# Optimization experiments

Hardware: AMD Instinct MI355X
Metric: run time of the kernel (lower is better)

Reference implementation:

```python
import jax, jax.numpy as jnp
import numpy as np

B, S, D, H = 4, 2048, 1024, 16
HD = D // H  # head dim = 64


def setup_inputs() -> dict:
    key = jax.random.key(0)
    ks = jax.random.split(key, 6)
    hidden_states = jax.random.normal(ks[0], (B, S, D), dtype=jnp.float32)
    attention_mask = jnp.zeros((B, S), dtype=bool)  # ignored by the module (set to None in forward)
    # RoPE cache: standard rotary angles per position
    inv_freq = 1.0 / (10000.0 ** (jnp.arange(0, HD, 2, dtype=jnp.float32) / HD))  # [HD/2]
    ang = jnp.arange(S, dtype=jnp.float32)[:, None] * inv_freq[None, :]  # [S, HD/2]
    ang = jnp.concatenate([ang, ang], axis=-1)  # [S, HD]
    rope_cos = jnp.cos(ang)
    rope_sin = jnp.sin(ang)
    scale = 1.0 / np.sqrt(D)
    Wq = jax.random.normal(ks[1], (D, D), dtype=jnp.float32) * scale
    Wk = jax.random.normal(ks[2], (D, D), dtype=jnp.float32) * scale
    Wv = jax.random.normal(ks[3], (D, D), dtype=jnp.float32) * scale
    return {"hidden_states": hidden_states, "attention_mask": attention_mask,
            "rope_cos": rope_cos, "rope_sin": rope_sin, "Wq": Wq, "Wk": Wk, "Wv": Wv}


def _rotate_half(x):
    x1, x2 = jnp.split(x, 2, axis=-1)
    return jnp.concatenate([-x2, x1], axis=-1)


def _apply_rope(x, cos, sin):
    # x: [B, H, S, HD]; cos/sin: [S, HD]
    return x * cos[None, None, :, :] + _rotate_half(x) * sin[None, None, :, :]


def reference(hidden_states, attention_mask, rope_cos, rope_sin, Wq, Wk, Wv):
    del attention_mask  # forward() sets attention_mask = None
    b, s, d = hidden_states.shape
    # QKV projections (nn.Linear: y = x @ W.T), split into heads -> [B, H, S, HD]
    def proj(W):
        y = jnp.einsum('bsd,ed->bse', hidden_states, W)
        return y.reshape(b, s, H, HD).transpose(0, 2, 1, 3)
    q = _apply_rope(proj(Wq), rope_cos, rope_sin)
    k = _apply_rope(proj(Wk), rope_cos, rope_sin)
    v = proj(Wv)
    # Softmax attention (non-causal, dropout_p=0)
    scores = jnp.einsum('bhqd,bhkd->bhqk', q, k) / np.sqrt(HD)
    probs = jax.nn.softmax(scores, axis=-1)
    ctx = jnp.einsum('bhqk,bhkd->bhqd', probs, v)
    # [B, H, S, HD] -> [B, S, D]
    return ctx.transpose(0, 2, 1, 3).reshape(b, s, d)
```

## Files before the change

kernel.cpp:

```cpp
#include <hip/hip_runtime.h>
#include <hip/hip_bf16.h>
#include <stdint.h>


typedef __attribute__((ext_vector_type(4)))  float    f32x4;
typedef __attribute__((ext_vector_type(16))) float    f32x16;
typedef __attribute__((ext_vector_type(8)))  __bf16   bf16x8;
typedef __attribute__((ext_vector_type(8)))  unsigned short ushort8;
typedef __attribute__((ext_vector_type(4)))  unsigned short ushort4v;
typedef __attribute__((ext_vector_type(4)))  uint32_t uint32x4;
typedef __attribute__((ext_vector_type(2)))  uint32_t uint32x2;

#define QSCALE 0.18033688011112042f
#define SMAX   16.0f

#define GL16(g, l)                                                            \
  __builtin_amdgcn_global_load_lds(                                           \
      (const __attribute__((address_space(1))) void*)(g),                     \
      (__attribute__((address_space(3))) void*)(l), 16, 0, 0)

__device__ inline unsigned short bf(float f) {
  return __builtin_bit_cast(unsigned short, (__bf16)f);
}
__device__ inline uint32_t cvtpk(float lo, float hi) {
  uint32_t r;
  asm volatile("v_cvt_pk_bf16_f32 %0, %1, %2" : "=v"(r) : "v"(lo), "v"(hi));
  return r;
}
__device__ inline bf16x8 ld16(const unsigned short* p) {
  return __builtin_bit_cast(bf16x8, *reinterpret_cast<const ushort8*>(p));
}

__global__ __launch_bounds__(256) void cvt_bf16(
    const float* __restrict__ X,
    const float* __restrict__ Wq, const float* __restrict__ Wk,
    const float* __restrict__ Wv,
    unsigned short* __restrict__ Xb, unsigned short* __restrict__ Wb)
{
  const int seg = blockIdx.y;
  const float* __restrict__ src = (seg == 0) ? X : (seg == 1) ? Wq : (seg == 2) ? Wk : Wv;
  unsigned short* __restrict__ dst = (seg == 0) ? Xb : Wb + (size_t)(seg - 1) * 1048576;
  const size_t n8 = (seg == 0) ? (size_t)1048576 : (size_t)131072;
  const size_t stride = (size_t)gridDim.x * 256;
  for (size_t i = blockIdx.x * 256 + threadIdx.x; i < n8; i += stride) {
    const float4 a = *reinterpret_cast<const float4*>(src + i * 8);
    const float4 b = *reinterpret_cast<const float4*>(src + i * 8 + 4);
    ushort8 o = { bf(a.x), bf(a.y), bf(a.z), bf(a.w), bf(b.x), bf(b.y), bf(b.z), bf(b.w) };
    *reinterpret_cast<ushort8*>(dst + i * 8) = o;
  }
}

__global__ __launch_bounds__(256) void qkv_gemm(
    const unsigned short* __restrict__ Xb, const unsigned short* __restrict__ Wb,
    const float* __restrict__ rc, const float* __restrict__ rs,
    unsigned short* __restrict__ Qb, unsigned short* __restrict__ Kb,
    unsigned short* __restrict__ VbT, int col0, int nheads_c, int gx)
{
  const int nwg = gridDim.x;
  const int q8 = nwg >> 3;
  int w = (blockIdx.x % 8) * q8 + blockIdx.x / 8;
  const int z = w / (gx * 64);
  const int r = w - z * gx * 64;
  const int brow = (r / gx) * 128;
  const int bcol = (r % gx) * 128;

  const unsigned short* __restrict__ Wz = Wb + (size_t)z * 1048576;

  const int tid  = threadIdx.x;
  const int lane = tid & 63;
  const int wid  = tid >> 6;
  const int wm = wid >> 1, wn = wid & 1;
  const int col16 = lane & 15, rowg = lane >> 4;

  __shared__ unsigned short As[128 * 32];
  __shared__ unsigned short Bs[128 * 32];

  f32x4 acc[4][4];
  #pragma unroll
  for (int m = 0; m < 4; ++m)
    #pragma unroll
    for (int n = 0; n < 4; ++n) acc[m][n] = (f32x4)0.f;

  const int srow = wid * 16 + (lane >> 2);
  const int scol = (lane & 3) * 8;
  const unsigned short* gA0 = Xb + (size_t)(brow + srow) * 1024 + scol;
  const unsigned short* gA1 = gA0 + (size_t)64 * 1024;
  const unsigned short* gB0 = Wz + (size_t)(col0 + bcol + srow) * 1024 + scol;
  const unsigned short* gB1 = gB0 + (size_t)64 * 1024;
  unsigned short* lA0 = &As[wid * 16 * 32];
  unsigned short* lA1 = &As[(64 + wid * 16) * 32];
  unsigned short* lB0 = &Bs[wid * 16 * 32];
  unsigned short* lB1 = &Bs[(64 + wid * 16) * 32];

  for (int k0 = 0; k0 < 1024; k0 += 32) {
    GL16(gA0 + k0, lA0);
    GL16(gA1 + k0, lA1);
    GL16(gB0 + k0, lB0);
    GL16(gB1 + k0, lB1);
    __syncthreads();

    bf16x8 af[4], bfv[4];
    #pragma unroll
    for (int m = 0; m < 4; ++m)
      af[m] = ld16(&As[(wm * 64 + m * 16 + col16) * 32 + rowg * 8]);
    #pragma unroll
    for (int n = 0; n < 4; ++n)
      bfv[n] = ld16(&Bs[(wn * 64 + n * 16 + col16) * 32 + rowg * 8]);
    #pragma unroll
    for (int m = 0; m < 4; ++m)
      #pragma unroll
      for (int n = 0; n < 4; ++n)
        acc[m][n] = __builtin_amdgcn_mfma_f32_16x16x32_bf16(af[m], bfv[n], acc[m][n], 0, 0, 0);
    __syncthreads();
  }

  #pragma unroll
  for (int m = 0; m < 4; ++m) {
    #pragma unroll
    for (int n = 0; n < 4; ++n) {
      const int e  = bcol + wn * 64 + n * 16 + col16;
      const int hl = e >> 6, hd = e & 63;
      if (z == 2) {
        const int row0 = brow + wm * 64 + m * 16 + rowg * 4;
        const int b = row0 >> 11, s0 = row0 & 2047;
        ushort4v o = { bf(acc[m][n][0]), bf(acc[m][n][1]), bf(acc[m][n][2]), bf(acc[m][n][3]) };
        *reinterpret_cast<ushort4v*>(
            VbT + ((size_t)(b * nheads_c + hl) * 64 + hd) * 2048 + s0) = o;
      } else {
        unsigned short* __restrict__ outp = (z == 0) ? Qb : Kb;
        #pragma unroll
        for (int j = 0; j < 4; ++j) {
          const int row = brow + wm * 64 + m * 16 + rowg * 4 + j;
          const int b = row >> 11, s = row & 2047;
          const float rot = (n < 2) ? -acc[m][n + 2][j] : acc[m][n - 2][j];
          float v = acc[m][n][j] * rc[s * 64 + hd] + rot * rs[s * 64 + hd];
          if (z == 0) v *= QSCALE;
          outp[((size_t)(b * nheads_c + hl) * 2048 + s) * 64 + hd] = bf(v);
        }
      }
    }
  }
}

__global__ __launch_bounds__(256) void attn(
    const unsigned short* __restrict__ Qb, const unsigned short* __restrict__ Kb,
    const unsigned short* __restrict__ VbT, float* __restrict__ out,
    int col0, int nheads_c)
{
  const int tid = threadIdx.x, lane = tid & 63, wq = tid >> 6;
  const int l31 = lane & 31, hi = lane >> 5;

  int wg = blockIdx.x;
  const int qx = (int)gridDim.x >> 3;
  wg = (wg & 7) * qx + (wg >> 3);
  const int bh = wg >> 4;
  const int q0 = (wg & 15) * 128;
  const int b = bh / nheads_c, hl = bh - b * nheads_c;
  const int hg = (col0 >> 6) + hl;
  const size_t base = (size_t)bh * 2048 * 64;

  __shared__ unsigned short L[4 * 4096];

  const int qrow = q0 + wq * 32 + l31;
  bf16x8 qf[4];
  #pragma unroll
  for (int ds = 0; ds < 4; ++ds)
    qf[ds] = ld16(Qb + base + (size_t)qrow * 64 + ds * 16 + hi * 8);

  ushort8 ov = { 0x3F80, 0x3F80, 0x3F80, 0x3F80, 0x3F80, 0x3F80, 0x3F80, 0x3F80 };
  const bf16x8 onesf = __builtin_bit_cast(bf16x8, ov);

  const int lr = lane >> 3, sw = (lane & 7) ^ lr;
  const int swz = l31 & 7;

  const unsigned short* kA[2][4];
  const unsigned short* vA[2][4];
  #pragma unroll
  for (int kb = 0; kb < 2; ++kb)
    #pragma unroll
    for (int ds = 0; ds < 4; ++ds)
      kA[kb][ds] = &L[(kb * 32 + l31) * 64 + (((ds * 2 + hi) ^ swz) * 8)];
  #pragma unroll
  for (int h2 = 0; h2 < 2; ++h2)
    #pragma unroll
    for (int ks = 0; ks < 4; ++ks)
      vA[h2][ks] = &L[8192 + (h2 * 32 + l31) * 64 + (((ks * 2 + hi) ^ swz) * 8)];

  f32x16 acc0 = (f32x16)0.f, acc1 = (f32x16)0.f, accL = (f32x16)0.f;

  GL16(Kb  + base + (size_t)(wq * 16 + lr) * 64 + sw * 8,       &L[(wq * 16) * 64]);
  GL16(Kb  + base + (size_t)(wq * 16 + 8 + lr) * 64 + sw * 8,   &L[(wq * 16 + 8) * 64]);
  GL16(VbT + base + (size_t)(wq * 16 + lr) * 2048 + sw * 8,     &L[8192 + (wq * 16) * 64]);
  GL16(VbT + base + (size_t)(wq * 16 + 8 + lr) * 2048 + sw * 8, &L[8192 + (wq * 16 + 8) * 64]);
  __syncthreads();

  const unsigned short* gk0 = Kb + base + (size_t)(64 + wq * 16 + lr) * 64 + sw * 8;
  const unsigned short* gk1 = gk0 + 8 * 64;
  const unsigned short* gv0 = VbT + base + (size_t)(wq * 16 + lr) * 2048 + 64 + sw * 8;
  const unsigned short* gv1 = gv0 + 8 * 2048;

#define PROC(BUF, KT)                                                          \
  {                                                                            \
    if ((KT) < 31) {                                                           \
      GL16(gk0, &L[((BUF) ^ 1) * 4096 + (wq * 16) * 64]);                      \
      GL16(gk1, &L[((BUF) ^ 1) * 4096 + (wq * 16 + 8) * 64]);                  \
      GL16(gv0, &L[8192 + ((BUF) ^ 1) * 4096 + (wq * 16) * 64]);               \
      GL16(gv1, &L[8192 + ((BUF) ^ 1) * 4096 + (wq * 16 + 8) * 64]);           \
      gk0 += 4096; gk1 += 4096; gv0 += 64; gv1 += 64;                          \
    }                                                                          \
    bf16x8 pa[4];                                                              \
    _Pragma("unroll")                                                          \
    for (int kb = 0; kb < 2; ++kb) {                                           \
      f32x16 s = (f32x16)(-SMAX);                                              \
      _Pragma("unroll")                                                        \
      for (int ds = 0; ds < 4; ++ds) {                                         \
        bf16x8 af = ld16(kA[kb][ds] + (BUF) * 4096);                           \
        s = __builtin_amdgcn_mfma_f32_32x32x16_bf16(af, qf[ds], s, 0, 0, 0);   \
      }                                                                        \
      float p[16];                                                             \
      _Pragma("unroll")                                                        \
      for (int rg = 0; rg < 16; ++rg) p[rg] = __builtin_exp2f(s[rg]);          \
      _Pragma("unroll")                                                        \
      for (int hf2 = 0; hf2 < 2; ++hf2) {                                      \
        uint32_t w0 = cvtpk(p[hf2 * 8 + 0], p[hf2 * 8 + 1]);                   \
        uint32_t w1 = cvtpk(p[hf2 * 8 + 2], p[hf2 * 8 + 3]);                   \
        uint32_t w2 = cvtpk(p[hf2 * 8 + 4], p[hf2 * 8 + 5]);                   \
        uint32_t w3 = cvtpk(p[hf2 * 8 + 6], p[hf2 * 8 + 7]);                   \
        uint32x2 a02 = __builtin_amdgcn_permlane32_swap(w0, w2, false, false); \
        uint32x2 a13 = __builtin_amdgcn_permlane32_swap(w1, w3, false, false); \
        uint32x4 d4 = { a02[0], a13[0], a02[1], a13[1] };                      \
        pa[kb * 2 + hf2] = __builtin_bit_cast(bf16x8, d4);                     \
      }                                                                        \
    }                                                                          \
    _Pragma("unroll")                                                          \
    for (int ks = 0; ks < 4; ++ks) {                                           \
      bf16x8 vf0 = ld16(vA[0][ks] + (BUF) * 4096);                             \
      bf16x8 vf1 = ld16(vA[1][ks] + (BUF) * 4096);                             \
      acc0 = __builtin_amdgcn_mfma_f32_32x32x16_bf16(pa[ks], vf0, acc0, 0, 0, 0); \
      acc1 = __builtin_amdgcn_mfma_f32_32x32x16_bf16(pa[ks], vf1, acc1, 0, 0, 0); \
      accL = __builtin_amdgcn_mfma_f32_32x32x16_bf16(pa[ks], onesf, accL, 0, 0, 0); \
    }                                                                          \
    __syncthreads();                                                           \
  }

  for (int t = 0; t < 16; ++t) {
    PROC(0, 2 * t);
    PROC(1, 2 * t + 1);
  }
#undef PROC

  #pragma unroll
  for (int rg = 0; rg < 16; ++rg) {
    const int qr = (rg & 3) + 8 * (rg >> 2) + 4 * hi;
    const float inv = 1.0f / accL[rg];
    const int s = q0 + wq * 32 + qr;
    float* o = out + ((size_t)(b * 2048 + s)) * 1024 + hg * 64 + l31;
    o[0]  = acc0[rg] * inv;
    o[32] = acc1[rg] * inv;
  }
}

extern "C" void kernel_launch(void* const* d_in, const int* in_sizes, int n_in,
                              void* d_out, int out_size, void* d_ws, size_t ws_size,
                              hipStream_t stream) {
  (void)in_sizes; (void)n_in; (void)out_size;
  const float* X  = (const float*)d_in[0];
  const float* rc = (const float*)d_in[2];
  const float* rs = (const float*)d_in[3];
  const float* Wq = (const float*)d_in[4];
  const float* Wk = (const float*)d_in[5];
  const float* Wv = (const float*)d_in[6];
  float* out = (float*)d_out;

  const size_t fixed = (size_t)2 * 8192 * 1024 + (size_t)3 * 2 * 1024 * 1024;
  int NC = 8;
  for (int nc = 1; nc <= 8; nc <<= 1) {
    size_t need = (size_t)3 * 2 * 8192 * (1024 / nc) + fixed;
    if (need <= ws_size) { NC = nc; break; }
  }
  const int CW = 1024 / NC;
  const int nheads_c = CW >> 6;
  const int nBH = 4 * nheads_c;
  const int gx = CW / 128;
  const size_t pc = (size_t)8192 * CW;

  unsigned short* Qb  = (unsigned short*)d_ws;
  unsigned short* Kb  = Qb + pc;
  unsigned short* VbT = Kb + pc;
  unsigned short* Xb  = VbT + pc;
  unsigned short* Wb  = Xb + (size_t)8192 * 1024;

  cvt_bf16<<<dim3(512, 4), 256, 0, stream>>>(X, Wq, Wk, Wv, Xb, Wb);

  for (int c = 0; c < NC; ++c) {
    const int col0 = c * CW;
    qkv_gemm<<<dim3(gx * 64 * 3), 256, 0, stream>>>(
        Xb, Wb, rc, rs, Qb, Kb, VbT, col0, nheads_c, gx);
    attn<<<dim3(16 * nBH), 256, 0, stream>>>(
        Qb, Kb, VbT, out, col0, nheads_c);
  }
}
```

Before: 190.6 us.

## Process two query tiles per wave and replace ones-MFMA row sums with scalar sums

The attention kernel now gives each wave 64 query rows, split into two 32-row sub-tiles, instead of 32. Each K/V fragment read from LDS therefore feeds twice as many MFMAs, and the grid shrinks by half. The softmax denominator is no longer computed with an extra MFMA against a ones vector. It is now summed in fp32 registers, reduced across the two half-waves with a shuffle, and staged through a small shared array. The P·V MFMAs are interleaved with the exp/convert work per k-slice. In exchange, register pressure rises and fewer workgroups run per chunk, which may hurt occupancy when heads are split into many column chunks.

Result: slower. 216.1 us (+13.4%).

```diff
diff --git a/kernel.cpp b/kernel.cpp
--- a/kernel.cpp
+++ b/kernel.cpp
@@ -153,22 +153,22 @@
   int wg = blockIdx.x;
   const int qx = (int)gridDim.x >> 3;
   wg = (wg & 7) * qx + (wg >> 3);
-  const int bh = wg >> 4;
-  const int q0 = (wg & 15) * 128;
+  const int bh = wg >> 3;
+  const int q0 = (wg & 7) * 256;
   const int b = bh / nheads_c, hl = bh - b * nheads_c;
   const int hg = (col0 >> 6) + hl;
   const size_t base = (size_t)bh * 2048 * 64;
 
   __shared__ unsigned short L[4 * 4096];
-
-  const int qrow = q0 + wq * 32 + l31;
-  bf16x8 qf[4];
-  #pragma unroll
-  for (int ds = 0; ds < 4; ++ds)
-    qf[ds] = ld16(Qb + base + (size_t)qrow * 64 + ds * 16 + hi * 8);
-
-  ushort8 ov = { 0x3F80, 0x3F80, 0x3F80, 0x3F80, 0x3F80, 0x3F80, 0x3F80, 0x3F80 };
-  const bf16x8 onesf = __builtin_bit_cast(bf16x8, ov);
+  __shared__ float Ls[256];
+
+  const int qb = q0 + wq * 64;
+  bf16x8 qfA[4], qfB[4];
+  #pragma unroll
+  for (int ds = 0; ds < 4; ++ds) {
+    qfA[ds] = ld16(Qb + base + (size_t)(qb + l31) * 64 + ds * 16 + hi * 8);
+    qfB[ds] = ld16(Qb + base + (size_t)(qb + 32 + l31) * 64 + ds * 16 + hi * 8);
+  }
 
   const int lr = lane >> 3, sw = (lane & 7) ^ lr;
   const int swz = l31 & 7;
@@ -186,7 +186,9 @@
     for (int ks = 0; ks < 4; ++ks)
       vA[h2][ks] = &L[8192 + (h2 * 32 + l31) * 64 + (((ks * 2 + hi) ^ swz) * 8)];
 
-  f32x16 acc0 = (f32x16)0.f, acc1 = (f32x16)0.f, accL = (f32x16)0.f;
+  f32x16 acc0A = (f32x16)0.f, acc1A = (f32x16)0.f;
+  f32x16 acc0B = (f32x16)0.f, acc1B = (f32x16)0.f;
+  float psA = 0.f, psB = 0.f;
 
   GL16(Kb  + base + (size_t)(wq * 16 + lr) * 64 + sw * 8,       &L[(wq * 16) * 64]);
   GL16(Kb  + base + (size_t)(wq * 16 + 8 + lr) * 64 + sw * 8,   &L[(wq * 16 + 8) * 64]);
@@ -208,37 +210,48 @@
       GL16(gv1, &L[8192 + ((BUF) ^ 1) * 4096 + (wq * 16 + 8) * 64]);           \
       gk0 += 4096; gk1 += 4096; gv0 += 64; gv1 += 64;                          \
     }                                                                          \
-    bf16x8 pa[4];                                                              \
     _Pragma("unroll")                                                          \
     for (int kb = 0; kb < 2; ++kb) {                                           \
-      f32x16 s = (f32x16)(-SMAX);                                              \
+      f32x16 sA = (f32x16)(-SMAX), sB = (f32x16)(-SMAX);                       \
       _Pragma("unroll")                                                        \
       for (int ds = 0; ds < 4; ++ds) {                                         \
         bf16x8 af = ld16(kA[kb][ds] + (BUF) * 4096);                           \
-        s = __builtin_amdgcn_mfma_f32_32x32x16_bf16(af, qf[ds], s, 0, 0, 0);   \
+        sA = __builtin_amdgcn_mfma_f32_32x32x16_bf16(af, qfA[ds], sA, 0, 0, 0); \
+        sB = __builtin_amdgcn_mfma_f32_32x32x16_bf16(af, qfB[ds], sB, 0, 0, 0); \
       }                                                                        \
-      float p[16];                                                             \
+      float pA[16], pB[16];                                                    \
       _Pragma("unroll")                                                        \
-      for (int rg = 0; rg < 16; ++rg) p[rg] = __builtin_exp2f(s[rg]);          \
+      for (int rg = 0; rg < 16; ++rg) {                                        \
+        pA[rg] = __builtin_exp2f(sA[rg]);                                      \
+        pB[rg] = __builtin_exp2f(sB[rg]);                                      \
+        psA += pA[rg]; psB += pB[rg];                                          \
+      }                                                                        \
       _Pragma("unroll")                                                        \
       for (int hf2 = 0; hf2 < 2; ++hf2) {                                      \
-        uint32_t w0 = cvtpk(p[hf2 * 8 + 0], p[hf2 * 8 + 1]);                   \
-        uint32_t w1 = cvtpk(p[hf2 * 8 + 2], p[hf2 * 8 + 3]);                   \
-        uint32_t w2 = cvtpk(p[hf2 * 8 + 4], p[hf2 * 8 + 5]);                   \
-        uint32_t w3 = cvtpk(p[hf2 * 8 + 6], p[hf2 * 8 + 7]);                   \
-        uint32x2 a02 = __builtin_amdgcn_permlane32_swap(w0, w2, false, false); \
-        uint32x2 a13 = __builtin_amdgcn_permlane32_swap(w1, w3, false, false); \
-        uint32x4 d4 = { a02[0], a13[0], a02[1], a13[1] };                      \
-        pa[kb * 2 + hf2] = __builtin_bit_cast(bf16x8, d4);                     \
+        uint32_t a0 = cvtpk(pA[hf2 * 8 + 0], pA[hf2 * 8 + 1]);                 \
+        uint32_t a1 = cvtpk(pA[hf2 * 8 + 2], pA[hf2 * 8 + 3]);                 \
+        uint32_t a2 = cvtpk(pA[hf2 * 8 + 4], pA[hf2 * 8 + 5]);                 \
+        uint32_t a3 = cvtpk(pA[hf2 * 8 + 6], pA[hf2 * 8 + 7]);                 \
+        uint32x2 aw02 = __builtin_amdgcn_permlane32_swap(a0, a2, false, false); \
+        uint32x2 aw13 = __builtin_amdgcn_permlane32_swap(a1, a3, false, false); \
+        uint32x4 dA = { aw02[0], aw13[0], aw02[1], aw13[1] };                  \
+        bf16x8 paA = __builtin_bit_cast(bf16x8, dA);                           \
+        uint32_t b0 = cvtpk(pB[hf2 * 8 + 0], pB[hf2 * 8 + 1]);                 \
+        uint32_t b1 = cvtpk(pB[hf2 * 8 + 2], pB[hf2 * 8 + 3]);                 \
+        uint32_t b2 = cvtpk(pB[hf2 * 8 + 4], pB[hf2 * 8 + 5]);                 \
+        uint32_t b3 = cvtpk(pB[hf2 * 8 + 6], pB[hf2 * 8 + 7]);                 \
+        uint32x2 bw02 = __builtin_amdgcn_permlane32_swap(b0, b2, false, false); \
+        uint32x2 bw13 = __builtin_amdgcn_permlane32_swap(b1, b3, false, false); \
+        uint32x4 dB = { bw02[0], bw13[0], bw02[1], bw13[1] };                  \
+        bf16x8 paB = __builtin_bit_cast(bf16x8, dB);                           \
+        const int ks = kb * 2 + hf2;                                           \
+        bf16x8 vf0 = ld16(vA[0][ks] + (BUF) * 4096);                           \
+        bf16x8 vf1 = ld16(vA[1][ks] + (BUF) * 4096);                           \
+        acc0A = __builtin_amdgcn_mfma_f32_32x32x16_bf16(paA, vf0, acc0A, 0, 0, 0); \
+        acc1A = __builtin_amdgcn_mfma_f32_32x32x16_bf16(paA, vf1, acc1A, 0, 0, 0); \
+        acc0B = __builtin_amdgcn_mfma_f32_32x32x16_bf16(paB, vf0, acc0B, 0, 0, 0); \
+        acc1B = __builtin_amdgcn_mfma_f32_32x32x16_bf16(paB, vf1, acc1B, 0, 0, 0); \
       }                                                                        \
-    }                                                                          \
-    _Pragma("unroll")                                                          \
-    for (int ks = 0; ks < 4; ++ks) {                                           \
-      bf16x8 vf0 = ld16(vA[0][ks] + (BUF) * 4096);                             \
-      bf16x8 vf1 = ld16(vA[1][ks] + (BUF) * 4096);                             \
-      acc0 = __builtin_amdgcn_mfma_f32_32x32x16_bf16(pa[ks], vf0, acc0, 0, 0, 0); \
-      acc1 = __builtin_amdgcn_mfma_f32_32x32x16_bf16(pa[ks], vf1, acc1, 0, 0, 0); \
-      accL = __builtin_amdgcn_mfma_f32_32x32x16_bf16(pa[ks], onesf, accL, 0, 0, 0); \
     }                                                                          \
     __syncthreads();                                                           \
   }
@@ -249,14 +262,23 @@
   }
 #undef PROC
 
+  psA += __shfl_xor(psA, 32);
+  psB += __shfl_xor(psB, 32);
+  if (hi == 0) {
+    Ls[wq * 64 + l31] = psA;
+    Ls[wq * 64 + 32 + l31] = psB;
+  }
   #pragma unroll
   for (int rg = 0; rg < 16; ++rg) {
     const int qr = (rg & 3) + 8 * (rg >> 2) + 4 * hi;
-    const float inv = 1.0f / accL[rg];
-    const int s = q0 + wq * 32 + qr;
-    float* o = out + ((size_t)(b * 2048 + s)) * 1024 + hg * 64 + l31;
-    o[0]  = acc0[rg] * inv;
-    o[32] = acc1[rg] * inv;
+    const float invA = 1.0f / Ls[wq * 64 + qr];
+    const float invB = 1.0f / Ls[wq * 64 + 32 + qr];
+    float* oA = out + ((size_t)(b * 2048 + qb + qr)) * 1024 + hg * 64 + l31;
+    float* oB = out + ((size_t)(b * 2048 + qb + 32 + qr)) * 1024 + hg * 64 + l31;
+    oA[0]  = acc0A[rg] * invA;
+    oA[32] = acc1A[rg] * invA;
+    oB[0]  = acc0B[rg] * invB;
+    oB[32] = acc1B[rg] * invB;
   }
 }
 
@@ -296,7 +318,7 @@
     const int col0 = c * CW;
     qkv_gemm<<<dim3(gx * 64 * 3), 256, 0, stream>>>(
         Xb, Wb, rc, rs, Qb, Kb, VbT, col0, nheads_c, gx);
-    attn<<<dim3(16 * nBH), 256, 0, stream>>>(
+    attn<<<dim3(8 * nBH), 256, 0, stream>>>(
         Qb, Kb, VbT, out, col0, nheads_c);
   }
 }
```
